# Optimization experiments

Measured on AMD Instinct MI355X. Metric: run time of the kernel, lower is better.

Reference implementation:

```python
import jax, jax.numpy as jnp
import numpy as np

N, C_IN, C_OUT, H, W = 16, 256, 256, 32, 32
K = 9  # 3x3 kernel


def setup_inputs() -> dict:
    key = jax.random.key(0)
    k1, k2, k3 = jax.random.split(key, 3)
    x = jax.random.normal(k1, (N, C_IN, H, W), dtype=jnp.float32)
    # offsets as produced upstream from anchors: (N, H*W, 18)
    offset = jax.random.normal(k2, (N, H * W, 2 * K), dtype=jnp.float32)
    # DeformConv weight (no bias), kaiming-ish scale
    weight = jax.random.normal(k3, (C_OUT, C_IN, 3, 3), dtype=jnp.float32) * 0.02
    return {"x": x, "offset": offset, "weight": weight}


def _deform_conv3x3(x, offset_nchw, weight):
    """DeformConv v1, kernel 3x3, stride 1, padding 1, dilation 1,
    groups=1, deformable_groups=1, zero padding outside borders."""
    n, c, h, w = x.shape
    o = weight.shape[0]
    # offset channel layout: (dy_k, dx_k) pairs for k = 0..8
    off = offset_nchw.reshape(n, K, 2, h, w)
    dy = off[:, :, 0]  # (N,K,H,W)
    dx = off[:, :, 1]
    ky = (jnp.arange(K) // 3 - 1).astype(x.dtype)  # kernel row offsets -1,0,1
    kx = (jnp.arange(K) % 3 - 1).astype(x.dtype)
    base_y = jnp.arange(h, dtype=x.dtype)[None, None, :, None]
    base_x = jnp.arange(w, dtype=x.dtype)[None, None, None, :]
    py = base_y + ky[None, :, None, None] + dy  # (N,K,H,W) sample rows
    px = base_x + kx[None, :, None, None] + dx  # (N,K,H,W) sample cols

    y0 = jnp.floor(py)
    x0 = jnp.floor(px)
    ly = py - y0  # fractional parts
    lx = px - x0

    x_flat = x.reshape(n, c, h * w)

    def corner(yi, xi, wgt):
        valid = (yi >= 0) & (yi <= h - 1) & (xi >= 0) & (xi <= w - 1)
        yc = jnp.clip(yi, 0, h - 1).astype(jnp.int32)
        xc = jnp.clip(xi, 0, w - 1).astype(jnp.int32)
        idx = (yc * w + xc).reshape(n, K * h * w)
        g = jax.vmap(lambda xf, i: xf[:, i])(x_flat, idx)  # (N,C,K*H*W)
        wv = (wgt * valid.astype(x.dtype)).reshape(n, 1, K * h * w)
        return g * wv

    val = (corner(y0, x0, (1 - ly) * (1 - lx))
           + corner(y0, x0 + 1, (1 - ly) * lx)
           + corner(y0 + 1, x0, ly * (1 - lx))
           + corner(y0 + 1, x0 + 1, ly * lx))
    val = val.reshape(n, c, K, h, w)  # sampled im2col columns
    return jnp.einsum('nckhw,ock->nohw', val, weight.reshape(o, c, K))


def reference(x, offset, weight):
    n, _, h, w = x.shape
    assert h * w == offset.shape[1]
    # AdaptiveConv.forward: (N, HW, 18) -> (N, 18, H, W)
    offset_nchw = jnp.transpose(offset, (0, 2, 1)).reshape(n, 2 * K, h, w)
    return _deform_conv3x3(x, offset_nchw, weight)
```

## Files before the change

kernel.cpp:

```cpp
#include <hip/hip_runtime.h>

#define NB   16
#define CIN  256
#define COUT 256
#define HH   32
#define WW   32
#define HW   1024
#define KK   9
#define CK   2304

typedef __bf16 bf16x8 __attribute__((ext_vector_type(8)));
typedef float  f32x4  __attribute__((ext_vector_type(4)));

__device__ __forceinline__ unsigned short f2bf(float f) {
    unsigned int u = __float_as_uint(f);
    u += 0x7FFFu + ((u >> 16) & 1u);
    return (unsigned short)(u >> 16);
}
__device__ __forceinline__ float bfhi(unsigned int u) {
    return __uint_as_float(u & 0xFFFF0000u);
}
__device__ __forceinline__ float bflo(unsigned int u) {
    return __uint_as_float(u << 16);
}

typedef const __attribute__((address_space(1))) void* gas_ptr;
typedef __attribute__((address_space(3))) void* las_ptr;

__device__ __forceinline__ void async16(const void* g, void* l) {
    __builtin_amdgcn_global_load_lds((gas_ptr)g, (las_ptr)l, 16, 0, 0);
}

__global__ __launch_bounds__(256) void wconv_kernel(const float* __restrict__ w,
                                                    unsigned short* __restrict__ wbf) {
    __shared__ float ls[CK];
    const int o = blockIdx.x;
    const float* wo = w + (size_t)o * CK;
#pragma unroll
    for (int i = threadIdx.x; i < CK; i += 256) ls[i] = wo[i];
    __syncthreads();
    unsigned short* dst = wbf + (size_t)o * CK;
#pragma unroll
    for (int i = threadIdx.x; i < CK; i += 256) {
        int k = i >> 8, c = i & 255;
        dst[i] = f2bf(ls[c * KK + k]);
    }
}

__global__ __launch_bounds__(256) void xt_kernel(const float* __restrict__ x,
                                                 unsigned short* __restrict__ xtb) {
    __shared__ float ls[64][65];
    const int c0  = blockIdx.x * 64;
    const int hw0 = blockIdx.y * 64;
    const int n   = blockIdx.z;
    const int t   = threadIdx.x;
    {
        int c = t >> 2, q = t & 3;
        const float* base = x + ((size_t)(n * CIN + c0 + c)) * HW + hw0 + q * 16;
#pragma unroll
        for (int j = 0; j < 16; ++j) ls[c][q * 16 + j] = base[j];
    }
    __syncthreads();
    {
        int hw = t >> 2, seg = (t & 3) * 16;
        unsigned int dw[8];
#pragma unroll
        for (int j = 0; j < 8; ++j) {
            float f0 = ls[seg + 2 * j][hw];
            float f1 = ls[seg + 2 * j + 1][hw];
            dw[j] = (unsigned)f2bf(f0) | ((unsigned)f2bf(f1) << 16);
        }
        uint4* dst = (uint4*)(xtb + ((size_t)(n * HW + hw0 + hw)) * CIN + c0 + seg);
        dst[0] = *(uint4*)&dw[0];
        dst[1] = *(uint4*)&dw[4];
    }
}

__global__ __launch_bounds__(256) void sample_kernel(const unsigned short* __restrict__ xtb,
                                                     const float* __restrict__ off,
                                                     unsigned short* __restrict__ valt) {
    const int wv   = threadIdx.x >> 6;
    const int lane = threadIdx.x & 63;
    const unsigned pbase = blockIdx.x * 32 + wv * 8;

#pragma unroll
    for (int i = 0; i < 8; ++i) {
        unsigned p = pbase + i;
        unsigned k = p % 9u;
        unsigned rest = p / 9u;
        unsigned hw = rest & 1023u;
        unsigned n  = rest >> 10;
        int h = (int)(hw >> 5), w = (int)(hw & 31);

        const float2* op2 = (const float2*)(off + ((size_t)(n * HW + hw)) * (2 * KK));
        float2 o = op2[k];
        float py = (float)(h + (int)(k / 3) - 1) + o.x;
        float px = (float)(w + (int)(k % 3) - 1) + o.y;
        float y0f = floorf(py), x0f = floorf(px);
        float ly = py - y0f, lx = px - x0f;
        int y0 = (int)y0f, x0 = (int)x0f;

        float wgt[4];
        int   ridx[4];
#pragma unroll
        for (int c2 = 0; c2 < 4; ++c2) {
            int yy = y0 + (c2 >> 1);
            int xx = x0 + (c2 & 1);
            float wy = (c2 >> 1) ? ly : 1.0f - ly;
            float wx = (c2 & 1) ? lx : 1.0f - lx;
            bool v = (yy >= 0) && (yy < HH) && (xx >= 0) && (xx < WW);
            wgt[c2] = v ? wy * wx : 0.0f;
            int yc = yy < 0 ? 0 : (yy > HH - 1 ? HH - 1 : yy);
            int xc = xx < 0 ? 0 : (xx > WW - 1 ? WW - 1 : xx);
            ridx[c2] = yc * WW + xc;
        }

        const uint2* base = (const uint2*)(xtb + (size_t)n * HW * CIN);
        uint2 d0 = base[(size_t)ridx[0] * 64 + lane];
        uint2 d1 = base[(size_t)ridx[1] * 64 + lane];
        uint2 d2 = base[(size_t)ridx[2] * 64 + lane];
        uint2 d3 = base[(size_t)ridx[3] * 64 + lane];

        float r0 = wgt[0] * bflo(d0.x) + wgt[1] * bflo(d1.x) + wgt[2] * bflo(d2.x) + wgt[3] * bflo(d3.x);
        float r1 = wgt[0] * bfhi(d0.x) + wgt[1] * bfhi(d1.x) + wgt[2] * bfhi(d2.x) + wgt[3] * bfhi(d3.x);
        float r2 = wgt[0] * bflo(d0.y) + wgt[1] * bflo(d1.y) + wgt[2] * bflo(d2.y) + wgt[3] * bflo(d3.y);
        float r3 = wgt[0] * bfhi(d0.y) + wgt[1] * bfhi(d1.y) + wgt[2] * bfhi(d2.y) + wgt[3] * bfhi(d3.y);

        uint2 outv;
        outv.x = (unsigned)f2bf(r0) | ((unsigned)f2bf(r1) << 16);
        outv.y = (unsigned)f2bf(r2) | ((unsigned)f2bf(r3) << 16);
        uint2* dst = (uint2*)(valt);
        dst[(size_t)(n * HW + hw) * 576 + k * 64 + lane] = outv;
    }
}

__global__ __launch_bounds__(256, 4) void gemm_kernel(const unsigned short* __restrict__ wbf,
                                                      const unsigned short* __restrict__ valt,
                                                      float* __restrict__ out) {
    __shared__ unsigned short As[64 * 64];
    __shared__ unsigned short Bs[64 * 64];

    const int tid  = threadIdx.x;
    const int wv   = tid >> 6;
    const int lane = tid & 63;
    const int quad = lane >> 4;
    const int l15  = lane & 15;
    const int wm   = wv & 1;
    const int wn   = wv >> 1;

    const int id = blockIdx.x;
    const int g  = id >> 5;
    const int r  = id & 31;
    const int o0 = (r >> 3) * 64;
    const int p  = g * 8 + (r & 7);
    const int hw0 = (p & 15) * 64;
    const int n   = p >> 4;

    const int srow   = lane >> 3;
    const int schunk = (lane & 7) ^ (srow & 7);

    const unsigned short* Ag = wbf + (size_t)o0 * CK;
    const unsigned short* Bg = valt + ((size_t)n * HW + hw0) * CK;

    f32x4 acc[2][2] = {};

    for (int ck0 = 0; ck0 < CK; ck0 += 64) {
        __syncthreads();
#pragma unroll
        for (int j = 0; j < 2; ++j) {
            int rb = wv * 16 + j * 8;
            async16(Ag + (size_t)(rb + srow) * CK + ck0 + schunk * 8, &As[rb * 64]);
            async16(Bg + (size_t)(rb + srow) * CK + ck0 + schunk * 8, &Bs[rb * 64]);
        }
        __syncthreads();

        bf16x8 af[2][2], bfr[2][2];
#pragma unroll
        for (int mi = 0; mi < 2; ++mi)
#pragma unroll
            for (int hh = 0; hh < 2; ++hh) {
                int row = wm * 32 + mi * 16 + l15;
                int ch  = (hh * 4 + quad) ^ (row & 7);
                af[mi][hh] = *(const bf16x8*)&As[row * 64 + ch * 8];
            }
#pragma unroll
        for (int ni = 0; ni < 2; ++ni)
#pragma unroll
            for (int hh = 0; hh < 2; ++hh) {
                int row = wn * 32 + ni * 16 + l15;
                int ch  = (hh * 4 + quad) ^ (row & 7);
                bfr[ni][hh] = *(const bf16x8*)&Bs[row * 64 + ch * 8];
            }
#pragma unroll
        for (int mi = 0; mi < 2; ++mi)
#pragma unroll
            for (int ni = 0; ni < 2; ++ni) {
                acc[mi][ni] = __builtin_amdgcn_mfma_f32_16x16x32_bf16(af[mi][0], bfr[ni][0], acc[mi][ni], 0, 0, 0);
                acc[mi][ni] = __builtin_amdgcn_mfma_f32_16x16x32_bf16(af[mi][1], bfr[ni][1], acc[mi][ni], 0, 0, 0);
            }
    }

    float* opnt = out + ((size_t)n * COUT + o0) * HW + hw0;
#pragma unroll
    for (int mi = 0; mi < 2; ++mi)
#pragma unroll
        for (int ni = 0; ni < 2; ++ni) {
            int col = wn * 32 + ni * 16 + l15;
#pragma unroll
            for (int rr = 0; rr < 4; ++rr) {
                int row = wm * 32 + mi * 16 + quad * 4 + rr;
                opnt[(size_t)row * HW + col] = acc[mi][ni][rr];
            }
        }
}

extern "C" void kernel_launch(void* const* d_in, const int* in_sizes, int n_in,
                              void* d_out, int out_size, void* d_ws, size_t ws_size,
                              hipStream_t stream) {
    const float* x   = (const float*)d_in[0];
    const float* off = (const float*)d_in[1];
    const float* wt  = (const float*)d_in[2];
    float* out = (float*)d_out;

    unsigned short* wbf  = (unsigned short*)d_ws;
    unsigned short* xtb  = (unsigned short*)((char*)d_ws + 1179648);
    unsigned short* valt = (unsigned short*)((char*)d_ws + 9568256);

    wconv_kernel<<<256, 256, 0, stream>>>(wt, wbf);
    xt_kernel<<<dim3(4, 16, 16), 256, 0, stream>>>(x, xtb);
    sample_kernel<<<4608, 256, 0, stream>>>(xtb, off, valt);
    gemm_kernel<<<1024, 256, 0, stream>>>(wbf, valt, out);
}
```

Baseline: 129.7 us.

## Fuse deformable bilinear sampling into the MFMA GEMM, removing im2col buffer

Replaces the separate sampling kernel and GEMM with one kernel. Each block computes all 256 output channels for 64 pixels. For each tap it gathers four bilinear corners from the transposed bf16 input, interpolates in registers and writes the tile straight into shared memory as the GEMM B operand. This removes the large intermediate im2col buffer write and re-read. The trade-off is a much smaller grid of 256 large blocks and more barriers per K-step, which may leave the GPU underoccupied and expose gather latency.

```diff
diff --git a/kernel.cpp b/kernel.cpp
--- a/kernel.cpp
+++ b/kernel.cpp
@@ -76,32 +76,47 @@
     }
 }
 
-__global__ __launch_bounds__(256) void sample_kernel(const unsigned short* __restrict__ xtb,
-                                                     const float* __restrict__ off,
-                                                     unsigned short* __restrict__ valt) {
-    const int wv   = threadIdx.x >> 6;
-    const int lane = threadIdx.x & 63;
-    const unsigned pbase = blockIdx.x * 32 + wv * 8;
-
-#pragma unroll
-    for (int i = 0; i < 8; ++i) {
-        unsigned p = pbase + i;
-        unsigned k = p % 9u;
-        unsigned rest = p / 9u;
-        unsigned hw = rest & 1023u;
-        unsigned n  = rest >> 10;
-        int h = (int)(hw >> 5), w = (int)(hw & 31);
-
-        const float2* op2 = (const float2*)(off + ((size_t)(n * HW + hw)) * (2 * KK));
-        float2 o = op2[k];
-        float py = (float)(h + (int)(k / 3) - 1) + o.x;
-        float px = (float)(w + (int)(k % 3) - 1) + o.y;
+__global__ __launch_bounds__(512, 2) void fused_kernel(const unsigned short* __restrict__ wbf,
+                                                       const unsigned short* __restrict__ xtb,
+                                                       const float* __restrict__ off,
+                                                       float* __restrict__ out) {
+    __shared__ unsigned short As[256 * 64];
+    __shared__ unsigned short Bs[64 * 64];
+
+    const int tid  = threadIdx.x;
+    const int wv   = tid >> 6;
+    const int lane = tid & 63;
+    const int quad = lane >> 4;
+    const int l15  = lane & 15;
+
+    const int hw_local = tid >> 3;
+    const int seg      = tid & 7;
+
+    const int id  = blockIdx.x;
+    const int hw0 = (id & 15) * 64;
+    const int n   = id >> 4;
+
+    const int hw = hw0 + hw_local;
+    const int h  = hw >> 5, w = hw & 31;
+
+    const int srow   = lane >> 3;
+    const int schunk = (lane & 7) ^ (srow & 7);
+
+    const uint4*  xb4  = (const uint4*)(xtb + (size_t)n * HW * CIN);
+    const float2* offp = (const float2*)(off + ((size_t)n * HW + hw) * (2 * KK));
+
+    f32x4 acc[2][4] = {};
+
+    for (int tap = 0; tap < KK; ++tap) {
+        float2 o = offp[tap];
+        float py = (float)(h + tap / 3 - 1) + o.x;
+        float px = (float)(w + tap % 3 - 1) + o.y;
         float y0f = floorf(py), x0f = floorf(px);
         float ly = py - y0f, lx = px - x0f;
         int y0 = (int)y0f, x0 = (int)x0f;
 
-        float wgt[4];
-        int   ridx[4];
+        float wg[4];
+        int   ix[4];
 #pragma unroll
         for (int c2 = 0; c2 < 4; ++c2) {
             int yy = y0 + (c2 >> 1);
@@ -109,106 +124,86 @@
             float wy = (c2 >> 1) ? ly : 1.0f - ly;
             float wx = (c2 & 1) ? lx : 1.0f - lx;
             bool v = (yy >= 0) && (yy < HH) && (xx >= 0) && (xx < WW);
-            wgt[c2] = v ? wy * wx : 0.0f;
+            wg[c2] = v ? wy * wx : 0.0f;
             int yc = yy < 0 ? 0 : (yy > HH - 1 ? HH - 1 : yy);
             int xc = xx < 0 ? 0 : (xx > WW - 1 ? WW - 1 : xx);
-            ridx[c2] = yc * WW + xc;
-        }
-
-        const uint2* base = (const uint2*)(xtb + (size_t)n * HW * CIN);
-        uint2 d0 = base[(size_t)ridx[0] * 64 + lane];
-        uint2 d1 = base[(size_t)ridx[1] * 64 + lane];
-        uint2 d2 = base[(size_t)ridx[2] * 64 + lane];
-        uint2 d3 = base[(size_t)ridx[3] * 64 + lane];
-
-        float r0 = wgt[0] * bflo(d0.x) + wgt[1] * bflo(d1.x) + wgt[2] * bflo(d2.x) + wgt[3] * bflo(d3.x);
-        float r1 = wgt[0] * bfhi(d0.x) + wgt[1] * bfhi(d1.x) + wgt[2] * bfhi(d2.x) + wgt[3] * bfhi(d3.x);
-        float r2 = wgt[0] * bflo(d0.y) + wgt[1] * bflo(d1.y) + wgt[2] * bflo(d2.y) + wgt[3] * bflo(d3.y);
-        float r3 = wgt[0] * bfhi(d0.y) + wgt[1] * bfhi(d1.y) + wgt[2] * bfhi(d2.y) + wgt[3] * bfhi(d3.y);
-
-        uint2 outv;
-        outv.x = (unsigned)f2bf(r0) | ((unsigned)f2bf(r1) << 16);
-        outv.y = (unsigned)f2bf(r2) | ((unsigned)f2bf(r3) << 16);
-        uint2* dst = (uint2*)(valt);
-        dst[(size_t)(n * HW + hw) * 576 + k * 64 + lane] = outv;
-    }
-}
-
-__global__ __launch_bounds__(256, 4) void gemm_kernel(const unsigned short* __restrict__ wbf,
-                                                      const unsigned short* __restrict__ valt,
-                                                      float* __restrict__ out) {
-    __shared__ unsigned short As[64 * 64];
-    __shared__ unsigned short Bs[64 * 64];
-
-    const int tid  = threadIdx.x;
-    const int wv   = tid >> 6;
-    const int lane = tid & 63;
-    const int quad = lane >> 4;
-    const int l15  = lane & 15;
-    const int wm   = wv & 1;
-    const int wn   = wv >> 1;
-
-    const int id = blockIdx.x;
-    const int g  = id >> 5;
-    const int r  = id & 31;
-    const int o0 = (r >> 3) * 64;
-    const int p  = g * 8 + (r & 7);
-    const int hw0 = (p & 15) * 64;
-    const int n   = p >> 4;
-
-    const int srow   = lane >> 3;
-    const int schunk = (lane & 7) ^ (srow & 7);
-
-    const unsigned short* Ag = wbf + (size_t)o0 * CK;
-    const unsigned short* Bg = valt + ((size_t)n * HW + hw0) * CK;
-
-    f32x4 acc[2][2] = {};
-
-    for (int ck0 = 0; ck0 < CK; ck0 += 64) {
-        __syncthreads();
-#pragma unroll
-        for (int j = 0; j < 2; ++j) {
-            int rb = wv * 16 + j * 8;
-            async16(Ag + (size_t)(rb + srow) * CK + ck0 + schunk * 8, &As[rb * 64]);
-            async16(Bg + (size_t)(rb + srow) * CK + ck0 + schunk * 8, &Bs[rb * 64]);
-        }
-        __syncthreads();
-
-        bf16x8 af[2][2], bfr[2][2];
-#pragma unroll
-        for (int mi = 0; mi < 2; ++mi)
-#pragma unroll
-            for (int hh = 0; hh < 2; ++hh) {
-                int row = wm * 32 + mi * 16 + l15;
-                int ch  = (hh * 4 + quad) ^ (row & 7);
-                af[mi][hh] = *(const bf16x8*)&As[row * 64 + ch * 8];
+            ix[c2] = yc * WW + xc;
+        }
+
+        uint4 cr[4][4];
+#pragma unroll
+        for (int c2 = 0; c2 < 4; ++c2) {
+            const uint4* rp = xb4 + (size_t)ix[c2] * 32 + seg;
+#pragma unroll
+            for (int s = 0; s < 4; ++s) cr[c2][s] = rp[s * 8];
+        }
+
+#pragma unroll
+        for (int s = 0; s < 4; ++s) {
+            __syncthreads();
+
+            const int ckb = tap * 256 + s * 64;
+#pragma unroll
+            for (int j = 0; j < 4; ++j) {
+                int rb = wv * 32 + j * 8;
+                async16(wbf + (size_t)(rb + srow) * CK + ckb + schunk * 8,
+                        &As[rb * 64]);
             }
-#pragma unroll
-        for (int ni = 0; ni < 2; ++ni)
-#pragma unroll
-            for (int hh = 0; hh < 2; ++hh) {
-                int row = wn * 32 + ni * 16 + l15;
-                int ch  = (hh * 4 + quad) ^ (row & 7);
-                bfr[ni][hh] = *(const bf16x8*)&Bs[row * 64 + ch * 8];
+
+            unsigned dw[4];
+            {
+                unsigned u0[4], u1[4], u2[4], u3[4];
+                *(uint4*)u0 = cr[0][s]; *(uint4*)u1 = cr[1][s];
+                *(uint4*)u2 = cr[2][s]; *(uint4*)u3 = cr[3][s];
+#pragma unroll
+                for (int d = 0; d < 4; ++d) {
+                    float lo = wg[0] * bflo(u0[d]) + wg[1] * bflo(u1[d])
+                             + wg[2] * bflo(u2[d]) + wg[3] * bflo(u3[d]);
+                    float hi = wg[0] * bfhi(u0[d]) + wg[1] * bfhi(u1[d])
+                             + wg[2] * bfhi(u2[d]) + wg[3] * bfhi(u3[d]);
+                    dw[d] = (unsigned)f2bf(lo) | ((unsigned)f2bf(hi) << 16);
+                }
             }
-#pragma unroll
-        for (int mi = 0; mi < 2; ++mi)
-#pragma unroll
-            for (int ni = 0; ni < 2; ++ni) {
-                acc[mi][ni] = __builtin_amdgcn_mfma_f32_16x16x32_bf16(af[mi][0], bfr[ni][0], acc[mi][ni], 0, 0, 0);
-                acc[mi][ni] = __builtin_amdgcn_mfma_f32_16x16x32_bf16(af[mi][1], bfr[ni][1], acc[mi][ni], 0, 0, 0);
-            }
-    }
-
-    float* opnt = out + ((size_t)n * COUT + o0) * HW + hw0;
+            *(uint4*)&Bs[hw_local * 64 + (seg ^ (hw_local & 7)) * 8] = *(uint4*)dw;
+
+            __syncthreads();
+
+            bf16x8 af[2][2], bfr[4][2];
+#pragma unroll
+            for (int mi = 0; mi < 2; ++mi)
+#pragma unroll
+                for (int hh = 0; hh < 2; ++hh) {
+                    int row = wv * 32 + mi * 16 + l15;
+                    int ch  = (hh * 4 + quad) ^ (row & 7);
+                    af[mi][hh] = *(const bf16x8*)&As[row * 64 + ch * 8];
+                }
+#pragma unroll
+            for (int ni = 0; ni < 4; ++ni)
+#pragma unroll
+                for (int hh = 0; hh < 2; ++hh) {
+                    int row = ni * 16 + l15;
+                    int ch  = (hh * 4 + quad) ^ (row & 7);
+                    bfr[ni][hh] = *(const bf16x8*)&Bs[row * 64 + ch * 8];
+                }
+#pragma unroll
+            for (int mi = 0; mi < 2; ++mi)
+#pragma unroll
+                for (int ni = 0; ni < 4; ++ni) {
+                    acc[mi][ni] = __builtin_amdgcn_mfma_f32_16x16x32_bf16(af[mi][0], bfr[ni][0], acc[mi][ni], 0, 0, 0);
+                    acc[mi][ni] = __builtin_amdgcn_mfma_f32_16x16x32_bf16(af[mi][1], bfr[ni][1], acc[mi][ni], 0, 0, 0);
+                }
+        }
+    }
+
+    float* opnt = out + (size_t)n * COUT * HW + hw0;
 #pragma unroll
     for (int mi = 0; mi < 2; ++mi)
 #pragma unroll
-        for (int ni = 0; ni < 2; ++ni) {
-            int col = wn * 32 + ni * 16 + l15;
+        for (int ni = 0; ni < 4; ++ni) {
+            int col = ni * 16 + l15;
 #pragma unroll
             for (int rr = 0; rr < 4; ++rr) {
-                int row = wm * 32 + mi * 16 + quad * 4 + rr;
+                int row = wv * 32 + mi * 16 + quad * 4 + rr;
                 opnt[(size_t)row * HW + col] = acc[mi][ni][rr];
             }
         }
@@ -222,12 +217,10 @@
     const float* wt  = (const float*)d_in[2];
     float* out = (float*)d_out;
 
-    unsigned short* wbf  = (unsigned short*)d_ws;
-    unsigned short* xtb  = (unsigned short*)((char*)d_ws + 1179648);
-    unsigned short* valt = (unsigned short*)((char*)d_ws + 9568256);
+    unsigned short* wbf = (unsigned short*)d_ws;
+    unsigned short* xtb = (unsigned short*)((char*)d_ws + 1179648);
 
     wconv_kernel<<<256, 256, 0, stream>>>(wt, wbf);
     xt_kernel<<<dim3(4, 16, 16), 256, 0, stream>>>(x, xtb);
-    sample_kernel<<<4608, 256, 0, stream>>>(xtb, off, valt);
-    gemm_kernel<<<1024, 256, 0, stream>>>(wbf, valt, out);
-}
+    fused_kernel<<<256, 512, 0, stream>>>(wbf, xtb, off, out);
+}
```

Result: slower. 132.3 us (+2.1%).
